# Kernel optimization log

Measured on AMD Instinct MI355X. Metric: run time of the kernel, lower is better.

Reference implementation:

```python
import jax, jax.numpy as jnp
import numpy as np

ENT_TYPES = 9
INNER_DIM = 64
BIG_NEG = 1e12


def _rope_tables(seq_len, dim, dtype):
    # sinusoidal_position_embedding: interleaved [sin, cos] of pos * 10000^(-2i/d)
    pos = jnp.arange(seq_len, dtype=jnp.float32)[:, None]            # [S,1]
    inv_freq = jnp.power(10000.0, -2.0 * jnp.arange(dim // 2, dtype=jnp.float32) / dim)
    ang = pos * inv_freq                                             # [S,D/2]
    emb = jnp.stack([jnp.sin(ang), jnp.cos(ang)], axis=-1).reshape(seq_len, dim)  # [S,D]
    cos_pos = jnp.repeat(emb[:, 1::2], 2, axis=-1).astype(dtype)     # [S,D]
    sin_pos = jnp.repeat(emb[:, ::2], 2, axis=-1).astype(dtype)      # [S,D]
    return cos_pos, sin_pos


def _rotate_half(x):
    # stack([-x[...,1::2], x[...,::2]], -1).reshape(x.shape)
    return jnp.stack([-x[..., 1::2], x[..., ::2]], axis=-1).reshape(x.shape)


def setup_inputs() -> dict:
    key = jax.random.key(0)
    k1, k2 = jax.random.split(key)
    B, S, H = 16, 512, 1024
    last_hidden_state = jax.random.normal(k1, (B, S, H), dtype=jnp.float32)
    padding_mask = jnp.ones((B, S), dtype=jnp.float32)
    W = jax.random.normal(k2, (H, ENT_TYPES * INNER_DIM * 2), dtype=jnp.float32) * (1.0 / np.sqrt(H))
    b = jnp.zeros((ENT_TYPES * INNER_DIM * 2,), dtype=jnp.float32)
    return {"last_hidden_state": last_hidden_state, "padding_mask": padding_mask, "W": W, "b": b}


def reference(last_hidden_state, padding_mask, W, b):
    B, S, _ = last_hidden_state.shape
    H, D = ENT_TYPES, INNER_DIM
    out = last_hidden_state @ W + b                 # [B,S,H*2D]
    out = out.reshape(B, S, H, 2 * D)
    qw, kw = out[..., :D], out[..., D:]             # [B,S,H,D]

    cos_pos, sin_pos = _rope_tables(S, D, qw.dtype)  # [S,D]
    cos_pos = cos_pos[None, :, None, :]
    sin_pos = sin_pos[None, :, None, :]
    qw = qw * cos_pos + _rotate_half(qw) * sin_pos
    kw = kw * cos_pos + _rotate_half(kw) * sin_pos

    logits = jnp.einsum('bmhd,bnhd->bhmn', qw, kw)   # [B,H,S,S]
    pad = padding_mask[:, None, None, :]             # mask over key dim
    logits = logits * pad - (1.0 - pad) * BIG_NEG
    tril = jnp.tril(jnp.ones((S, S), dtype=logits.dtype), -1)
    logits = logits - tril * BIG_NEG
    return logits / jnp.sqrt(jnp.asarray(D, dtype=logits.dtype))
```

## Files before the change

kernel.cpp:

```cpp
#include <hip/hip_runtime.h>

#define EN 9
#define DD 64
#define SS 512
#define HH 1024
#define NOUT 1152

typedef float f32x4 __attribute__((ext_vector_type(4)));

#define GPTR(p) ((const __attribute__((address_space(1))) void*)(p))
#define LPTR(p) ((__attribute__((address_space(3))) void*)(p))

__device__ inline int pk4_fp8(float a, float b, float c, float d) {
  int v = __builtin_amdgcn_cvt_pk_fp8_f32(a, b, 0, false);
  v = __builtin_amdgcn_cvt_pk_fp8_f32(c, d, v, true);
  return v;
}

__device__ inline unsigned short f2bf(float f) {
  unsigned int u = __float_as_uint(f);
  return (unsigned short)((u + 0x7FFFu + ((u >> 16) & 1u)) >> 16);
}

__global__ __launch_bounds__(256) void prep_kernel(
    const float* __restrict__ W, const float* __restrict__ X,
    unsigned char* __restrict__ Wf8, unsigned char* __restrict__ Xf8,
    float* __restrict__ ctab, float* __restrict__ stab) {
  if (blockIdx.x < 288u) {
    __shared__ float t[64][65];
    const int k0 = (blockIdx.x / 18) * 64;
    const int n0 = (blockIdx.x % 18) * 64;
    const int r = threadIdx.x >> 6;
    const int c = threadIdx.x & 63;
#pragma unroll
    for (int i = 0; i < 16; ++i) {
      const int kk = (i << 2) + r;
      t[kk][c] = W[(size_t)(k0 + kk) * NOUT + n0 + c];
    }
    __syncthreads();
#pragma unroll
    for (int i = 0; i < 2; ++i) {
      const int p = (i << 8) + threadIdx.x;
      const int n = p >> 3, cc = p & 7;
      const int kk = cc << 3;
      const int lo = pk4_fp8(t[kk][n], t[kk + 1][n], t[kk + 2][n], t[kk + 3][n]);
      const int hi =
          pk4_fp8(t[kk + 4][n], t[kk + 5][n], t[kk + 6][n], t[kk + 7][n]);
      const int gn = n0 + n;
      int2 v;
      v.x = lo;
      v.y = hi;
      *(int2*)(Wf8 + (size_t)gn * HH + k0 + ((cc ^ (gn & 7)) << 3)) = v;
    }
  } else if (blockIdx.x < 304u) {
    const int bt = blockIdx.x - 288;
#pragma unroll
    for (int j = 0; j < 4; ++j) {
      const int id = bt * 1024 + j * 256 + threadIdx.x;
      const int s = id >> 5, i = id & 31;
      const float freq = expf(-(float)(2 * i) * (9.210340371976184f / 64.0f));
      const float ang = (float)s * freq;
      ctab[id] = cosf(ang);
      stab[id] = sinf(ang);
    }
  } else {
    const int bt = blockIdx.x - 304;
#pragma unroll
    for (int j = 0; j < 4; ++j) {
      const int C = bt * 1024 + (j << 8) + threadIdx.x;
      const int row = C >> 7, c = C & 127;
      const float4 v0 = *(const float4*)(X + (size_t)C * 8);
      const float4 v1 = *(const float4*)(X + (size_t)C * 8 + 4);
      int2 v;
      v.x = pk4_fp8(v0.x, v0.y, v0.z, v0.w);
      v.y = pk4_fp8(v1.x, v1.y, v1.z, v1.w);
      *(int2*)(Xf8 + (size_t)row * HH + ((c >> 3) << 6) +
               (((c ^ row) & 7) << 3)) = v;
    }
  }
}

__global__ __launch_bounds__(256, 4) void proj_rope_kernel(
    const unsigned char* __restrict__ Xf8, const unsigned char* __restrict__ Wf8,
    const float* __restrict__ bias, const float* __restrict__ ctab,
    const float* __restrict__ stab, unsigned char* __restrict__ QK) {
  __shared__ __align__(16) unsigned char sm[32768];
  const int tid = threadIdx.x;
  const int lane = tid & 63;
  const int wid = tid >> 6;
  const int wr = wid >> 1, wc = wid & 1;
  const int f = blockIdx.x;
  const int wkr = (f & 7) * 72 + (f >> 3);
  const int m0 = (wkr / 9) << 7;
  const int n0 = (wkr % 9) << 7;

  f32x4 acc[4][4];
#pragma unroll
  for (int i = 0; i < 4; ++i)
#pragma unroll
    for (int j = 0; j < 4; ++j) acc[i][j] = (f32x4){0.f, 0.f, 0.f, 0.f};

#define STAGE(BUF, KT)                                                       \
  {                                                                          \
    const int kt_ = (KT);                                                    \
    unsigned char* dst_ = sm + (BUF)*16384;                                  \
    _Pragma("unroll") for (int it = 0; it < 2; ++it) {                       \
      const int u_ = (it << 8) + tid;                                        \
      const int r_ = u_ >> 2, g_ = u_ & 3;                                   \
      __builtin_amdgcn_global_load_lds(                                      \
          GPTR(Xf8 + (size_t)(m0 + r_) * HH + kt_ + (g_ << 4)),              \
          LPTR(dst_ + (((it << 8) + (wid << 6)) << 4)), 16, 0, 0);           \
      __builtin_amdgcn_global_load_lds(                                      \
          GPTR(Wf8 + (size_t)(n0 + r_) * HH + kt_ + (g_ << 4)),              \
          LPTR(dst_ + 8192 + (((it << 8) + (wid << 6)) << 4)), 16, 0, 0);    \
    }                                                                        \
  }

#define COMPUTE(BUF)                                                         \
  {                                                                          \
    const unsigned char* smc_ = sm + (BUF)*16384;                            \
    __builtin_amdgcn_s_setprio(1);                                           \
    _Pragma("unroll") for (int kb = 0; kb < 2; ++kb) {                       \
      long aL[4], bL[4];                                                     \
      const int c8 = (kb << 2) + (lane >> 4);                                \
      _Pragma("unroll") for (int i = 0; i < 4; ++i) {                        \
        const int ra = (wr << 6) + (i << 4) + (lane & 15);                   \
        aL[i] = *(const long*)(smc_ + (ra << 6) + (((c8 ^ ra) & 7) << 3));   \
        const int rb = (wc << 6) + (i << 4) + (lane & 15);                   \
        bL[i] = *(const long*)(smc_ + 8192 + (rb << 6) +                     \
                               (((c8 ^ rb) & 7) << 3));                      \
      }                                                                      \
      _Pragma("unroll") for (int mi = 0; mi < 4; ++mi)                       \
          _Pragma("unroll") for (int ni = 0; ni < 4; ++ni) acc[mi][ni] =     \
          __builtin_amdgcn_mfma_f32_16x16x32_fp8_fp8(aL[mi], bL[ni],         \
                                                     acc[mi][ni], 0, 0, 0);  \
    }                                                                        \
    __builtin_amdgcn_s_setprio(0);                                           \
  }

  STAGE(0, 0)
#pragma unroll 1
  for (int t = 0; t < 15; ++t) {
    STAGE((t + 1) & 1, (t + 1) << 6)
    asm volatile("s_waitcnt vmcnt(4)" ::: "memory");
    __builtin_amdgcn_s_barrier();
    __builtin_amdgcn_sched_barrier(0);
    COMPUTE(t & 1)
    __builtin_amdgcn_sched_barrier(0);
    __builtin_amdgcn_s_barrier();
  }
  asm volatile("s_waitcnt vmcnt(0)" ::: "memory");
  __builtin_amdgcn_s_barrier();
  __builtin_amdgcn_sched_barrier(0);
  COMPUTE(1)

  __syncthreads();
  float* scr = (float*)sm;
  const int erow = tid >> 3;
  const int ec8 = (tid & 7) << 1;
#pragma unroll
  for (int mi = 0; mi < 4; ++mi) {
#pragma unroll
    for (int ni = 0; ni < 4; ++ni) {
      const int col = (wc << 6) + (ni << 4) + (lane & 15);
#pragma unroll
      for (int r = 0; r < 4; ++r) {
        const int row = (wr << 4) + ((lane >> 4) << 2) + r;
        scr[row * 132 + col] = acc[mi][ni][r];
      }
    }
    __syncthreads();
    const int m = m0 + ((erow >> 4) << 6) + (mi << 4) + (erow & 15);
    const int s = m & (SS - 1);
    const int bb = m >> 9;
#pragma unroll
    for (int sl = 0; sl < 2; ++sl) {
      const int c8 = ec8 + sl;
      const int ncol = c8 << 3;
      const int n = n0 + ncol;
      const int h = n >> 7;
      const int t = (n >> 6) & 1;
      const int d0 = n & 63;
      const float scale = (t == 0) ? 0.125f : 1.0f;
      const float4 va = *(const float4*)&scr[erow * 132 + ncol];
      const float4 vb = *(const float4*)&scr[erow * 132 + ncol + 4];
      const float4 bia = *(const float4*)&bias[n];
      const float4 bib = *(const float4*)&bias[n + 4];
      const float4 cs = *(const float4*)&ctab[(s << 5) + (d0 >> 1)];
      const float4 sn = *(const float4*)&stab[(s << 5) + (d0 >> 1)];
      const float e0 = va.x + bia.x, o0 = va.y + bia.y;
      const float e1 = va.z + bia.z, o1 = va.w + bia.w;
      const float e2 = vb.x + bib.x, o2 = vb.y + bib.y;
      const float e3 = vb.z + bib.z, o3 = vb.w + bib.w;
      int2 ov;
      ov.x = pk4_fp8((e0 * cs.x - o0 * sn.x) * scale,
                     (o0 * cs.x + e0 * sn.x) * scale,
                     (e1 * cs.y - o1 * sn.y) * scale,
                     (o1 * cs.y + e1 * sn.y) * scale);
      ov.y = pk4_fp8((e2 * cs.z - o2 * sn.z) * scale,
                     (o2 * cs.z + e2 * sn.z) * scale,
                     (e3 * cs.w - o3 * sn.w) * scale,
                     (o3 * cs.w + e3 * sn.w) * scale);
      const int cswz = (((d0 >> 3) ^ (s & 7)) << 3);
      *(int2*)(QK + (((size_t)(bb * EN + h) * 2 + t) * SS + s) * DD + cswz) =
          ov;
    }
    __syncthreads();
  }
}

__global__ __launch_bounds__(256, 4) void logits_kernel(
    const unsigned char* __restrict__ QK, const float* __restrict__ pmask,
    float* __restrict__ out) {
  __shared__ __align__(16) unsigned char sm[16384];
  const int tid = threadIdx.x;
  const int lane = tid & 63;
  const int wid = tid >> 6;
  const int wr = wid >> 1, wc = wid & 1;
  const int f = blockIdx.x;
  const int wkr = (f & 7) * 288 + (f >> 3);
  const int bh = wkr >> 4;
  const int bb = bh / EN;
  const int tm = (wkr >> 2) & 3, tn = wkr & 3;
  const int mq0 = tm << 7, nk0 = tn << 7;
  const unsigned char* Qb = QK + (size_t)bh * 2 * SS * DD;
  const unsigned char* Kb = Qb + SS * DD;

#pragma unroll
  for (int it = 0; it < 2; ++it) {
    const int u = (it << 8) + tid;
    const int r = u >> 2, g = u & 3;
    __builtin_amdgcn_global_load_lds(
        GPTR(Qb + (size_t)(mq0 + r) * DD + (g << 4)),
        LPTR(sm + (((it << 8) + (wid << 6)) << 4)), 16, 0, 0);
    __builtin_amdgcn_global_load_lds(
        GPTR(Kb + (size_t)(nk0 + r) * DD + (g << 4)),
        LPTR(sm + 8192 + (((it << 8) + (wid << 6)) << 4)), 16, 0, 0);
  }
  __syncthreads();

  f32x4 acc[4][4];
#pragma unroll
  for (int i = 0; i < 4; ++i)
#pragma unroll
    for (int j = 0; j < 4; ++j) acc[i][j] = (f32x4){0.f, 0.f, 0.f, 0.f};

#pragma unroll
  for (int kb = 0; kb < 2; ++kb) {
    long aL[4], bL[4];
    const int c8 = (kb << 2) + (lane >> 4);
#pragma unroll
    for (int i = 0; i < 4; ++i) {
      const int ra = (wr << 6) + (i << 4) + (lane & 15);
      aL[i] = *(const long*)(sm + (ra << 6) + (((c8 ^ ra) & 7) << 3));
      const int rb = (wc << 6) + (i << 4) + (lane & 15);
      bL[i] = *(const long*)(sm + 8192 + (rb << 6) + (((c8 ^ rb) & 7) << 3));
    }
#pragma unroll
    for (int mi = 0; mi < 4; ++mi)
#pragma unroll
      for (int ni = 0; ni < 4; ++ni)
        acc[mi][ni] = __builtin_amdgcn_mfma_f32_16x16x32_fp8_fp8(
            aL[mi], bL[ni], acc[mi][ni], 0, 0, 0);
  }

#pragma unroll
  for (int mi = 0; mi < 4; ++mi) {
#pragma unroll
    for (int ni = 0; ni < 4; ++ni) {
      const int n = nk0 + (wc << 6) + (ni << 4) + (lane & 15);
      const float pd = pmask[bb * SS + n];
      const float sub = (1.0f - pd) * 1.25e11f;
#pragma unroll
      for (int r = 0; r < 4; ++r) {
        const int m = mq0 + (wr << 6) + (mi << 4) + ((lane >> 4) << 2) + r;
        float v = acc[mi][ni][r] * pd - sub;
        if (m > n) v -= 1.25e11f;
        out[((size_t)bh * SS + m) * SS + n] = v;
      }
    }
  }
}

extern "C" void kernel_launch(void* const* d_in, const int* in_sizes, int n_in,
                              void* d_out, int out_size, void* d_ws,
                              size_t ws_size, hipStream_t stream) {
  const float* X = (const float*)d_in[0];
  const float* pm = (const float*)d_in[1];
  const float* W = (const float*)d_in[2];
  const float* bias = (const float*)d_in[3];
  float* out = (float*)d_out;
  unsigned char* ws = (unsigned char*)d_ws;
  unsigned char* QK = ws;
  unsigned char* Wf8 = ws + 9437184;
  float* ctab = (float*)(ws + 10616832);
  float* stab = (float*)(ws + 10682368);
  unsigned char* Xf8 = ws + 10747904;

  prep_kernel<<<dim3(1328), dim3(256), 0, stream>>>(W, X, Wf8, Xf8, ctab, stab);
  proj_rope_kernel<<<dim3(576), dim3(256), 0, stream>>>(Xf8, Wf8, bias, ctab,
                                                        stab, QK);
  logits_kernel<<<dim3(2304), dim3(256), 0, stream>>>(QK, pm, out);
}
```

Baseline: 62.72 us.

## Use single-wave 64x64 projection tiles with more blocks and no barriers

The projection+RoPE GEMM moves from 256-thread blocks computing 128x128 tiles to 64-thread single-wavefront blocks computing 64x64 tiles, launched as 2304 blocks instead of 576. Because one wave owns each block, the per-iteration s_barriers are removed and only a vmcnt wait orders the double-buffered LDS loads. The aim is more blocks to spread across CUs and no block-level sync stalls. The cost is lower operand reuse per tile: each block reads its own X and W slices, so global/L2 traffic for the GEMM roughly doubles.

```diff
diff --git a/kernel.cpp b/kernel.cpp
--- a/kernel.cpp
+++ b/kernel.cpp
@@ -15,11 +15,6 @@
   int v = __builtin_amdgcn_cvt_pk_fp8_f32(a, b, 0, false);
   v = __builtin_amdgcn_cvt_pk_fp8_f32(c, d, v, true);
   return v;
-}
-
-__device__ inline unsigned short f2bf(float f) {
-  unsigned int u = __float_as_uint(f);
-  return (unsigned short)((u + 0x7FFFu + ((u >> 16) & 1u)) >> 16);
 }
 
 __global__ __launch_bounds__(256) void prep_kernel(
@@ -80,19 +75,20 @@
   }
 }
 
-__global__ __launch_bounds__(256, 4) void proj_rope_kernel(
+__global__ __launch_bounds__(64) void proj_rope_kernel(
     const unsigned char* __restrict__ Xf8, const unsigned char* __restrict__ Wf8,
     const float* __restrict__ bias, const float* __restrict__ ctab,
     const float* __restrict__ stab, unsigned char* __restrict__ QK) {
-  __shared__ __align__(16) unsigned char sm[32768];
-  const int tid = threadIdx.x;
-  const int lane = tid & 63;
-  const int wid = tid >> 6;
-  const int wr = wid >> 1, wc = wid & 1;
+  __shared__ __align__(16) unsigned char sm[16384];
+  const int lane = threadIdx.x;
   const int f = blockIdx.x;
-  const int wkr = (f & 7) * 72 + (f >> 3);
-  const int m0 = (wkr / 9) << 7;
-  const int n0 = (wkr % 9) << 7;
+  const int wkr = (f & 7) * 288 + (f >> 3);
+  const int m0 = (wkr / 18) << 6;
+  const int nt = wkr % 18;
+  const int n0 = nt << 6;
+  const int hh = n0 >> 7;
+  const int tt = (n0 >> 6) & 1;
+  const float scale = (tt == 0) ? 0.125f : 1.0f;
 
   f32x4 acc[4][4];
 #pragma unroll
@@ -100,94 +96,87 @@
 #pragma unroll
     for (int j = 0; j < 4; ++j) acc[i][j] = (f32x4){0.f, 0.f, 0.f, 0.f};
 
-#define STAGE(BUF, KT)                                                       \
-  {                                                                          \
-    const int kt_ = (KT);                                                    \
-    unsigned char* dst_ = sm + (BUF)*16384;                                  \
-    _Pragma("unroll") for (int it = 0; it < 2; ++it) {                       \
-      const int u_ = (it << 8) + tid;                                        \
-      const int r_ = u_ >> 2, g_ = u_ & 3;                                   \
-      __builtin_amdgcn_global_load_lds(                                      \
-          GPTR(Xf8 + (size_t)(m0 + r_) * HH + kt_ + (g_ << 4)),              \
-          LPTR(dst_ + (((it << 8) + (wid << 6)) << 4)), 16, 0, 0);           \
-      __builtin_amdgcn_global_load_lds(                                      \
-          GPTR(Wf8 + (size_t)(n0 + r_) * HH + kt_ + (g_ << 4)),              \
-          LPTR(dst_ + 8192 + (((it << 8) + (wid << 6)) << 4)), 16, 0, 0);    \
-    }                                                                        \
-  }
-
-#define COMPUTE(BUF)                                                         \
-  {                                                                          \
-    const unsigned char* smc_ = sm + (BUF)*16384;                            \
-    __builtin_amdgcn_s_setprio(1);                                           \
-    _Pragma("unroll") for (int kb = 0; kb < 2; ++kb) {                       \
-      long aL[4], bL[4];                                                     \
-      const int c8 = (kb << 2) + (lane >> 4);                                \
-      _Pragma("unroll") for (int i = 0; i < 4; ++i) {                        \
-        const int ra = (wr << 6) + (i << 4) + (lane & 15);                   \
-        aL[i] = *(const long*)(smc_ + (ra << 6) + (((c8 ^ ra) & 7) << 3));   \
-        const int rb = (wc << 6) + (i << 4) + (lane & 15);                   \
-        bL[i] = *(const long*)(smc_ + 8192 + (rb << 6) +                     \
-                               (((c8 ^ rb) & 7) << 3));                      \
-      }                                                                      \
-      _Pragma("unroll") for (int mi = 0; mi < 4; ++mi)                       \
-          _Pragma("unroll") for (int ni = 0; ni < 4; ++ni) acc[mi][ni] =     \
-          __builtin_amdgcn_mfma_f32_16x16x32_fp8_fp8(aL[mi], bL[ni],         \
-                                                     acc[mi][ni], 0, 0, 0);  \
-    }                                                                        \
-    __builtin_amdgcn_s_setprio(0);                                           \
+  const int sr = lane >> 2;
+  const int sg = (lane & 3) << 4;
+
+#define STAGE(BUF, KT)                                                      \
+  {                                                                         \
+    const int kt_ = (KT);                                                   \
+    unsigned char* dst_ = sm + (BUF)*8192;                                  \
+    _Pragma("unroll") for (int i = 0; i < 4; ++i) {                         \
+      __builtin_amdgcn_global_load_lds(                                     \
+          GPTR(Xf8 + (size_t)(m0 + (i << 4) + sr) * HH + kt_ + sg),         \
+          LPTR(dst_ + (i << 10)), 16, 0, 0);                                \
+    }                                                                       \
+    _Pragma("unroll") for (int i = 0; i < 4; ++i) {                         \
+      __builtin_amdgcn_global_load_lds(                                     \
+          GPTR(Wf8 + (size_t)(n0 + (i << 4) + sr) * HH + kt_ + sg),         \
+          LPTR(dst_ + 4096 + (i << 10)), 16, 0, 0);                         \
+    }                                                                       \
+  }
+
+#define COMPUTE(BUF)                                                        \
+  {                                                                         \
+    const unsigned char* smc_ = sm + (BUF)*8192;                            \
+    __builtin_amdgcn_s_setprio(1);                                          \
+    _Pragma("unroll") for (int kb = 0; kb < 2; ++kb) {                      \
+      long aL[4], bL[4];                                                    \
+      const int c8 = (kb << 2) + (lane >> 4);                               \
+      _Pragma("unroll") for (int i = 0; i < 4; ++i) {                       \
+        const int ra = (i << 4) + (lane & 15);                              \
+        aL[i] = *(const long*)(smc_ + (ra << 6) + (((c8 ^ ra) & 7) << 3));  \
+        bL[i] = *(const long*)(smc_ + 4096 + (ra << 6) +                    \
+                               (((c8 ^ ra) & 7) << 3));                     \
+      }                                                                     \
+      _Pragma("unroll") for (int mi = 0; mi < 4; ++mi)                      \
+          _Pragma("unroll") for (int ni = 0; ni < 4; ++ni) acc[mi][ni] =    \
+          __builtin_amdgcn_mfma_f32_16x16x32_fp8_fp8(aL[mi], bL[ni],        \
+                                                     acc[mi][ni], 0, 0, 0); \
+    }                                                                       \
+    __builtin_amdgcn_s_setprio(0);                                          \
   }
 
   STAGE(0, 0)
 #pragma unroll 1
   for (int t = 0; t < 15; ++t) {
     STAGE((t + 1) & 1, (t + 1) << 6)
-    asm volatile("s_waitcnt vmcnt(4)" ::: "memory");
-    __builtin_amdgcn_s_barrier();
+    asm volatile("s_waitcnt vmcnt(8)" ::: "memory");
     __builtin_amdgcn_sched_barrier(0);
     COMPUTE(t & 1)
-    __builtin_amdgcn_sched_barrier(0);
-    __builtin_amdgcn_s_barrier();
   }
   asm volatile("s_waitcnt vmcnt(0)" ::: "memory");
-  __builtin_amdgcn_s_barrier();
   __builtin_amdgcn_sched_barrier(0);
   COMPUTE(1)
 
   __syncthreads();
   float* scr = (float*)sm;
-  const int erow = tid >> 3;
-  const int ec8 = (tid & 7) << 1;
+  const int erow = lane >> 2;
+  const int ecol = (lane & 3) << 4;
 #pragma unroll
   for (int mi = 0; mi < 4; ++mi) {
 #pragma unroll
     for (int ni = 0; ni < 4; ++ni) {
-      const int col = (wc << 6) + (ni << 4) + (lane & 15);
+      const int col = (ni << 4) + (lane & 15);
 #pragma unroll
       for (int r = 0; r < 4; ++r) {
-        const int row = (wr << 4) + ((lane >> 4) << 2) + r;
-        scr[row * 132 + col] = acc[mi][ni][r];
+        const int row = ((lane >> 4) << 2) + r;
+        scr[row * 68 + col] = acc[mi][ni][r];
       }
     }
     __syncthreads();
-    const int m = m0 + ((erow >> 4) << 6) + (mi << 4) + (erow & 15);
+    const int m = m0 + (mi << 4) + erow;
     const int s = m & (SS - 1);
     const int bb = m >> 9;
 #pragma unroll
     for (int sl = 0; sl < 2; ++sl) {
-      const int c8 = ec8 + sl;
-      const int ncol = c8 << 3;
+      const int ncol = ecol + (sl << 3);
       const int n = n0 + ncol;
-      const int h = n >> 7;
-      const int t = (n >> 6) & 1;
-      const int d0 = n & 63;
-      const float scale = (t == 0) ? 0.125f : 1.0f;
-      const float4 va = *(const float4*)&scr[erow * 132 + ncol];
-      const float4 vb = *(const float4*)&scr[erow * 132 + ncol + 4];
+      const float4 va = *(const float4*)&scr[erow * 68 + ncol];
+      const float4 vb = *(const float4*)&scr[erow * 68 + ncol + 4];
       const float4 bia = *(const float4*)&bias[n];
       const float4 bib = *(const float4*)&bias[n + 4];
-      const float4 cs = *(const float4*)&ctab[(s << 5) + (d0 >> 1)];
-      const float4 sn = *(const float4*)&stab[(s << 5) + (d0 >> 1)];
+      const float4 cs = *(const float4*)&ctab[(s << 5) + (ncol >> 1)];
+      const float4 sn = *(const float4*)&stab[(s << 5) + (ncol >> 1)];
       const float e0 = va.x + bia.x, o0 = va.y + bia.y;
       const float e1 = va.z + bia.z, o1 = va.w + bia.w;
       const float e2 = vb.x + bib.x, o2 = vb.y + bib.y;
@@ -201,8 +190,8 @@
                      (o2 * cs.z + e2 * sn.z) * scale,
                      (e3 * cs.w - o3 * sn.w) * scale,
                      (o3 * cs.w + e3 * sn.w) * scale);
-      const int cswz = (((d0 >> 3) ^ (s & 7)) << 3);
-      *(int2*)(QK + (((size_t)(bb * EN + h) * 2 + t) * SS + s) * DD + cswz) =
+      const int cswz = (((ncol >> 3) ^ (s & 7)) << 3);
+      *(int2*)(QK + (((size_t)(bb * EN + hh) * 2 + tt) * SS + s) * DD + cswz) =
           ov;
     }
     __syncthreads();
@@ -298,7 +287,7 @@
   unsigned char* Xf8 = ws + 10747904;
 
   prep_kernel<<<dim3(1328), dim3(256), 0, stream>>>(W, X, Wf8, Xf8, ctab, stab);
-  proj_rope_kernel<<<dim3(576), dim3(256), 0, stream>>>(Xf8, Wf8, bias, ctab,
+  proj_rope_kernel<<<dim3(2304), dim3(64), 0, stream>>>(Xf8, Wf8, bias, ctab,
                                                         stab, QK);
   logits_kernel<<<dim3(2304), dim3(256), 0, stream>>>(QK, pm, out);
 }
```

Measured after the change: 69.25 us. 10.4% more time.
